# Performance work log

Hardware: AMD Instinct MI355X
Metric: run time of the kernel (lower is better)

Reference implementation:

```python
import jax, jax.numpy as jnp
import numpy as np

S = 1024        # img_size
RADIUS = 512    # number of radial bins
WEIGHT = 1.0


def _bin_idx():
    # Matches torch.meshgrid(arange(-s/2, s/2), ..., indexing='ij') with +0.5 offsets.
    xs = jnp.arange(-S / 2, S / 2, dtype=jnp.float32)
    d = jnp.sqrt((xs[:, None] + 0.5) ** 2 + (xs[None, :] + 0.5) ** 2)  # [S, S]
    # Bin edges are integers 0..RADIUS, so mask (d>=r)&(d<r+1) == (floor(d)==r).
    idx = jnp.floor(d).astype(jnp.int32)
    # Pixels with d >= RADIUS fall in no mask -> overflow bucket RADIUS (dropped later).
    return jnp.where(d < RADIUS, idx, RADIUS).reshape(-1)  # [S*S]


def _power_spec(image):
    ft = jnp.fft.fft2(image)                 # [B, C, S, S] complex
    return jnp.fft.fftshift(jnp.abs(ft) ** 2, axes=(-2, -1))


def _radial_power_spec(ps2d, idx):
    B, C = ps2d.shape[0], ps2d.shape[1]
    flat = ps2d.reshape(B * C, S * S)
    # Histogram reduction: O(S*S) instead of the original O(RADIUS*S*S) dense mask multiply.
    seg = jax.vmap(lambda v: jax.ops.segment_sum(v, idx, num_segments=RADIUS + 1))(flat)
    rad = seg[:, :RADIUS] / (S * S)          # mean over (H, W), drop overflow bucket
    return rad.reshape(B, C, RADIUS).sum(axis=1)  # sum over channel dim


def setup_inputs() -> dict:
    key = jax.random.key(0)
    k1, k2 = jax.random.split(key)
    output = jax.random.normal(k1, (16, 1, S, S), dtype=jnp.float32)
    target = jax.random.normal(k2, (16, 1, S, S), dtype=jnp.float32)
    return {"output": output, "target": target}


def reference(output, target):
    idx = _bin_idx()
    ps_out = _radial_power_spec(_power_spec(output), idx)   # [B, RADIUS]
    ps_tgt = _radial_power_spec(_power_spec(target), idx)   # [B, RADIUS]
    return jnp.mean(jnp.abs(ps_out - ps_tgt)) * WEIGHT
```

## Files before the change

### kernel.cpp

```cpp
#include <hip/hip_runtime.h>
#include <math.h>

#define S 1024
#define RADIUS 512
#define NIMG 32
#define PBX 129

__device__ __forceinline__ float2 cmul(float2 a, float2 b) {
    return make_float2(a.x * b.x - a.y * b.y, a.x * b.y + a.y * b.x);
}
__device__ __forceinline__ float2 cadd(float2 a, float2 b) { return make_float2(a.x + b.x, a.y + b.y); }
__device__ __forceinline__ float2 csub(float2 a, float2 b) { return make_float2(a.x - b.x, a.y - b.y); }

__device__ const float2 C16[8] = {
    {1.0f, 0.0f},
    {0.92387953251128674f, -0.38268343236508978f},
    {0.70710678118654757f, -0.70710678118654746f},
    {0.38268343236508984f, -0.92387953251128674f},
    {0.0f, -1.0f},
    {-0.38268343236508973f, -0.92387953251128674f},
    {-0.70710678118654746f, -0.70710678118654757f},
    {-0.92387953251128663f, -0.38268343236508989f},
};
__device__ const float2 C8T[4] = {
    {1.0f, 0.0f},
    {0.70710678118654757f, -0.70710678118654746f},
    {0.0f, -1.0f},
    {-0.70710678118654746f, -0.70710678118654757f},
};
__device__ const float2 W512T[8] = {
    {1.0f, 0.0f},
    {0.99992470183914454f, -0.012271538285719925f},
    {0.99969881869620425f, -0.024541228522912288f},
    {0.99932238458834954f, -0.036807222941358832f},
    {0.99879545620517241f, -0.049067674327418015f},
    {0.99811811290014918f, -0.061320736302208578f},
    {0.99729045667869021f, -0.073564563599667426f},
    {0.99631261218277800f, -0.085797312344439894f},
};
__device__ const float2 W64T[8] = {
    {1.0f, 0.0f},
    {0.99518472667219693f, -0.098017140329560604f},
    {0.98078528040323044f, -0.19509032201612825f},
    {0.95694033573220886f, -0.29028467725446233f},
    {0.92387953251128674f, -0.38268343236508978f},
    {0.88192126434835505f, -0.47139673682599764f},
    {0.83146961230254524f, -0.55557023301960218f},
    {0.77301045336273699f, -0.63439328416364549f},
};
__device__ const float2 W128P[8] = {
    {1.0f, 0.0f},
    {0.99879545620517241f, -0.049067674327418015f},
    {0.99518472667219693f, -0.098017140329560604f},
    {0.98917650996478101f, -0.14673047445536175f},
    {0.98078528040323044f, -0.19509032201612825f},
    {0.97003125319454397f, -0.24298017990326390f},
    {0.95694033573220886f, -0.29028467725446233f},
    {0.94154406518302081f, -0.33688985339222005f},
};
__device__ const float2 W1024P[8] = {
    {1.0f, 0.0f},
    {0.99998117528260111f, -0.0061358846491544753f},
    {0.99992470183914454f, -0.012271538285719925f},
    {0.99983058179582340f, -0.018406729905804820f},
    {0.99969881869620425f, -0.024541228522912288f},
    {0.99952941750109314f, -0.030674803176636626f},
    {0.99932238458834954f, -0.036807222941358832f},
    {0.99907772775264536f, -0.042938256934940820f},
};

__device__ __forceinline__ void fft16(float2 r[16], float2 T) {
    float2 tc[8];
    #pragma unroll
    for (int u = 0; u < 8; ++u) tc[u] = cmul(T, C16[u]);
    #pragma unroll
    for (int u = 0; u < 8; ++u) {
        float2 a = r[u], b = r[u + 8];
        r[u] = cadd(a, b);
        r[u + 8] = cmul(csub(a, b), tc[u]);
    }
    T = cmul(T, T);
    #pragma unroll
    for (int u = 0; u < 4; ++u) tc[u] = cmul(T, C16[2 * u]);
    #pragma unroll
    for (int g = 0; g < 2; ++g)
        #pragma unroll
        for (int u = 0; u < 4; ++u) {
            int lo = g * 8 + u;
            float2 a = r[lo], b = r[lo + 4];
            r[lo] = cadd(a, b);
            r[lo + 4] = cmul(csub(a, b), tc[u]);
        }
    T = cmul(T, T);
    #pragma unroll
    for (int u = 0; u < 2; ++u) tc[u] = cmul(T, C16[4 * u]);
    #pragma unroll
    for (int g = 0; g < 4; ++g)
        #pragma unroll
        for (int u = 0; u < 2; ++u) {
            int lo = g * 4 + u;
            float2 a = r[lo], b = r[lo + 2];
            r[lo] = cadd(a, b);
            r[lo + 2] = cmul(csub(a, b), tc[u]);
        }
    T = cmul(T, T);
    #pragma unroll
    for (int g = 0; g < 8; ++g) {
        int lo = g * 2;
        float2 a = r[lo], b = r[lo + 1];
        r[lo] = cadd(a, b);
        r[lo + 1] = cmul(csub(a, b), T);
    }
}

__device__ __forceinline__ void fft8(float2 r[8], float2 T) {
    float2 tc[4];
    #pragma unroll
    for (int u = 0; u < 4; ++u) tc[u] = cmul(T, C8T[u]);
    #pragma unroll
    for (int u = 0; u < 4; ++u) {
        float2 a = r[u], b = r[u + 4];
        r[u] = cadd(a, b);
        r[u + 4] = cmul(csub(a, b), tc[u]);
    }
    T = cmul(T, T);
    #pragma unroll
    for (int u = 0; u < 2; ++u) tc[u] = cmul(T, C8T[2 * u]);
    #pragma unroll
    for (int g = 0; g < 2; ++g)
        #pragma unroll
        for (int u = 0; u < 2; ++u) {
            int lo = g * 4 + u;
            float2 a = r[lo], b = r[lo + 2];
            r[lo] = cadd(a, b);
            r[lo + 2] = cmul(csub(a, b), tc[u]);
        }
    T = cmul(T, T);
    #pragma unroll
    for (int g = 0; g < 4; ++g) {
        int lo = g * 2;
        float2 a = r[lo], b = r[lo + 1];
        r[lo] = cadd(a, b);
        r[lo + 1] = cmul(csub(a, b), T);
    }
}

__device__ __forceinline__ void fft_last2(float2 r[16], int c) {
    #pragma unroll
    for (int m = 0; m < 16; ++m) {
        float vx = __shfl_xor(r[m].x, 2, 64);
        float vy = __shfl_xor(r[m].y, 2, 64);
        if (c & 2) {
            float dx = vx - r[m].x, dy = vy - r[m].y;
            if (c & 1) { r[m].x = dy; r[m].y = -dx; }
            else       { r[m].x = dx; r[m].y = dy; }
        } else {
            r[m].x += vx; r[m].y += vy;
        }
    }
    #pragma unroll
    for (int m = 0; m < 16; ++m) {
        float vx = __shfl_xor(r[m].x, 1, 64);
        float vy = __shfl_xor(r[m].y, 1, 64);
        if (c & 1) { r[m].x = vx - r[m].x; r[m].y = vy - r[m].y; }
        else       { r[m].x += vx; r[m].y += vy; }
    }
}

__device__ __forceinline__ int A1x(int n) {
    int j = n >> 6;
    return (n & ~63) | ((n & 63) ^ (j << 2));
}

__device__ __forceinline__ int bitrev3(int x) {
    return ((x & 1) << 2) | (x & 2) | ((x >> 2) & 1);
}

__global__ __launch_bounds__(512)
void fft_rows(const float* __restrict__ outp, const float* __restrict__ tgtp,
              float2* __restrict__ WpT, int imgBase) {
    __shared__ float2 buf[8 * 1024];
    const int t = threadIdx.x;
    const int w = t >> 6, tau = t & 63;
    const int yy = blockIdx.x * 8 + w;
    const int i = blockIdx.y, g = imgBase + i;
    const float* img = (g < 16 ? outp : tgtp) + (size_t)(g & 15) * S * S;
    const float* r0 = img + (size_t)(2 * yy) * S;
    const float* r1 = r0 + S;

    float2 r[16];
    #pragma unroll
    for (int j = 0; j < 16; ++j) r[j] = make_float2(r0[64 * j + tau], r1[64 * j + tau]);

    float2 T = cmul(W128P[tau >> 3], W1024P[tau & 7]);
    fft16(r, T);

    float2* mybuf = buf + (w << 10);
    #pragma unroll
    for (int j = 0; j < 16; ++j) mybuf[A1x(64 * j + tau)] = r[j];
    const int b = tau >> 2, c = tau & 3;
    #pragma unroll
    for (int m = 0; m < 16; ++m) r[m] = mybuf[(b << 6) + 4 * (m ^ b) + c];

    fft16(r, W64T[c]);
    fft_last2(r, c);

    #pragma unroll
    for (int m = 0; m < 16; ++m) {
        int n = (b << 6) + 4 * m + c;
        int k = (int)(__brev((unsigned)n) >> 22);
        mybuf[k ^ (w << 1)] = r[m];
    }
    __syncthreads();

    const int yy0 = blockIdx.x * 8;
    float2* dst = WpT + (size_t)i * 512 * 1024;
    #pragma unroll
    for (int q = 0; q < 16; ++q) {
        int idx = q * 512 + t;
        int uu = idx >> 3, wv = idx & 7;
        float2 val = buf[(wv << 10) | (uu ^ (wv << 1))];
        dst[(size_t)uu * 512 + yy0 + wv] = val;
    }
}

__global__ __launch_bounds__(512, 4)
void fft_cols_bin2(const float2* __restrict__ WpT, float* __restrict__ partial, int imgBase) {
    __shared__ float2 tbuf[8 * 512];
    __shared__ float pref[512];
    __shared__ float cws[8];
    __shared__ float cwx[8];
    const int t = threadIdx.x;
    const int w = t >> 6, tau = t & 63;
    const int i = blockIdx.y, g = imgBase + i;
    const int l = w >> 1;
    const int u = blockIdx.x * 4 + l;
    const int setb = w & 1;
    const bool active = (u <= 512);

    const int b3 = tau >> 3, lam = tau & 7;
    float2 X[8];
    float2* mb = tbuf + (w << 9);

    if (active) {
        const float2* Wimg = WpT + (size_t)i * 512 * 1024;
        const int mu = (1024 - u) & 1023;
        const float2* rowA = Wimg + (size_t)u * 512;
        const float2* rowM = Wimg + (size_t)mu * 512;

        #pragma unroll
        for (int j = 0; j < 8; ++j) {
            float2 A = rowA[64 * j + tau];
            float2 M = rowM[64 * j + tau];
            X[j] = (setb == 0)
                 ? make_float2(0.5f * (A.x + M.x), 0.5f * (A.y - M.y))
                 : make_float2(0.5f * (A.y + M.y), 0.5f * (M.x - A.x));
        }

        fft8(X, cmul(W64T[b3], W512T[lam]));

        #pragma unroll
        for (int j = 0; j < 8; ++j) mb[(j << 6) | (tau ^ (j << 3) ^ j)] = X[j];
        #pragma unroll
        for (int c = 0; c < 8; ++c) X[c] = mb[(b3 << 6) | (((c ^ b3) << 3) | (lam ^ b3))];

        fft8(X, W64T[lam]);

        #pragma unroll
        for (int c = 0; c < 8; ++c) mb[(b3 << 6) | (((c ^ b3) << 3) | (lam ^ b3))] = X[c];
        #pragma unroll
        for (int d = 0; d < 8; ++d) X[d] = mb[(b3 << 6) | (((lam ^ b3) << 3) | (d ^ b3))];

        fft8(X, make_float2(1.0f, 0.0f));

        const int base9 = 8 * bitrev3(lam) + bitrev3(b3);
        #pragma unroll
        for (int d = 0; d < 8; ++d) {
            mb[(bitrev3(d) << 6) + base9] = X[d];
        }
    }
    __syncthreads();

    float p[8];
    if (active) {
        const float2* b0 = tbuf + ((w & ~1) << 9);
        const float2* b1 = tbuf + ((w | 1) << 9);
        const float2 Wtau = cmul(W128P[tau >> 3], W1024P[tau & 7]);
        #pragma unroll
        for (int m = 0; m < 8; ++m) {
            const int f = tau + 64 * m;
            float2 x0 = b0[f];
            float2 x1 = b1[f];
            float2 Wf = cmul(Wtau, C16[m]);
            float2 wx = cmul(Wf, x1);
            float2 G = (setb == 0) ? cadd(x0, wx)
                                   : csub(x0, wx);
            p[m] = G.x * G.x + G.y * G.y;
        }
    }
    __syncthreads();

    float* Prow = (float*)tbuf;
    if (active) {
        #pragma unroll
        for (int m = 0; m < 8; ++m) {
            const int v = tau + 64 * m + (setb << 9);
            Prow[(l << 10) + v] = p[m];
        }
    }
    __syncthreads();

    const int r = t;
    const float r2  = (float)(r * r);
    const float r12 = (float)((r + 1) * (r + 1));
    float acc = 0.0f;

    for (int rowi = 0; rowi < 8; ++rowi) {
        const int ll = rowi >> 1;
        const int mir = rowi & 1;
        const int uu = blockIdx.x * 4 + ll;
        const bool valid = (uu <= 512) && (!mir || (uu >= 1 && uu <= 511));
        float F = 0.0f;
        if (valid) {
            const float* PR = Prow + (ll << 10);
            F = mir ? (PR[t + 1] + PR[(1024 - t) & 1023])
                    : (PR[t] + PR[1023 - t]);
        }
        float s = F;
        #pragma unroll
        for (int off = 1; off < 64; off <<= 1) {
            float n = __shfl_up(s, off, 64);
            if (tau >= off) s += n;
        }
        pref[t] = s;
        if (tau == 63) cws[w] = s;
        __syncthreads();
        if (t < 8) {
            float x = 0.0f;
            #pragma unroll
            for (int j = 0; j < 8; ++j) {
                if (j < t) x += cws[j];
            }
            cwx[t] = x;
        }
        __syncthreads();
        if (valid) {
            const float cuv = mir ? ((float)uu - 0.5f)
                                  : ((uu < 512) ? ((float)uu + 0.5f) : 511.5f);
            const float cu2 = cuv * cuv;
            const float Bv = r12 - cu2;
            if (Bv > 0.0f) {
                const float Av = r2 - cu2;
                float cvlo = (Av > 0.0f) ? sqrtf(Av) : 0.0f;
                float cvhi = sqrtf(Bv);
                int vlo = (int)ceilf(cvlo - 0.5f);
                int vhi = (int)ceilf(cvhi - 0.5f);
                if (vhi > 512) vhi = 512;
                if (vlo < 0) vlo = 0;
                if (vhi > vlo) {
                    float hi = pref[vhi - 1] + cwx[(vhi - 1) >> 6];
                    float lo = (vlo > 0) ? (pref[vlo - 1] + cwx[(vlo - 1) >> 6]) : 0.0f;
                    acc += hi - lo;
                }
            }
        }
        __syncthreads();
    }
    partial[(((size_t)g * PBX) + blockIdx.x) * 512 + t] = acc;
}

__global__ __launch_bounds__(512)
void reduce_partials(const float* __restrict__ partial, float* __restrict__ rad) {
    const int g = blockIdx.x;
    const int t = threadIdx.x;
    const float* p = partial + (size_t)g * PBX * 512;
    float s = 0.0f;
    for (int b = 0; b < PBX; ++b) s += p[(size_t)b * 512 + t];
    rad[(size_t)g * 512 + t] = s;
}

__global__ __launch_bounds__(256)
void final_loss(const float* __restrict__ rad, float* __restrict__ out) {
    __shared__ float red[256];
    const int t = threadIdx.x;
    float acc = 0.0f;
    for (int i = t; i < 16 * RADIUS; i += 256) {
        int bb = i >> 9;
        int rr = i & (RADIUS - 1);
        float o = rad[(size_t)bb * RADIUS + rr];
        float gg = rad[(size_t)(bb + 16) * RADIUS + rr];
        acc += fabsf(o - gg);
    }
    red[t] = acc;
    __syncthreads();
    for (int off = 128; off > 0; off >>= 1) {
        if (t < off) red[t] += red[t + off];
        __syncthreads();
    }
    if (t == 0) {
        out[0] = red[0] / ((float)S * (float)S) / (16.0f * (float)RADIUS);
    }
}

extern "C" void kernel_launch(void* const* d_in, const int* in_sizes, int n_in,
                              void* d_out, int out_size, void* d_ws, size_t ws_size,
                              hipStream_t stream) {
    const float* outp = (const float*)d_in[0];
    const float* tgtp = (const float*)d_in[1];
    float* dout = (float*)d_out;

    char* ws = (char*)d_ws;
    float* rad = (float*)ws;
    const size_t partBytes = (size_t)NIMG * PBX * 512 * sizeof(float);
    float* partial = (float*)(ws + 65536);
    float2* WpT = (float2*)(ws + 65536 + partBytes);
    const size_t perImg = (size_t)512 * 1024 * sizeof(float2);
    size_t used = 65536 + partBytes;
    size_t avail = (ws_size > used) ? (ws_size - used) : 0;
    int chunk = (int)(avail / perImg);
    if (chunk > NIMG) chunk = NIMG;
    if (chunk < 1) chunk = 1;

    for (int base = 0; base < NIMG; base += chunk) {
        int c = (NIMG - base < chunk) ? (NIMG - base) : chunk;
        fft_rows<<<dim3(64, c), 512, 0, stream>>>(outp, tgtp, WpT, base);
        fft_cols_bin2<<<dim3(PBX, c), 512, 0, stream>>>(WpT, partial, base);
    }

    reduce_partials<<<NIMG, 512, 0, stream>>>(partial, rad);
    final_loss<<<1, 256, 0, stream>>>(rad, dout);
}
```

Measured before the change: 171.5 us.

## Halve fft_rows shared memory via two-phase transposes to raise occupancy

Shrinks the row-FFT kernel's shared buffer from 8K to 4K float2 by performing both in-kernel transposes in two halves, and declares four blocks per CU in launch bounds. The intent is to lift occupancy limited by shared-memory size and improve latency hiding. It adds extra barriers and an extra 8-element register array, which may increase register pressure or cause spills under the tighter launch bound.

```diff
diff --git a/kernel.cpp b/kernel.cpp
--- a/kernel.cpp
+++ b/kernel.cpp
@@ -167,19 +167,14 @@
     }
 }
 
-__device__ __forceinline__ int A1x(int n) {
-    int j = n >> 6;
-    return (n & ~63) | ((n & 63) ^ (j << 2));
-}
-
 __device__ __forceinline__ int bitrev3(int x) {
     return ((x & 1) << 2) | (x & 2) | ((x >> 2) & 1);
 }
 
-__global__ __launch_bounds__(512)
+__global__ __launch_bounds__(512, 4)
 void fft_rows(const float* __restrict__ outp, const float* __restrict__ tgtp,
               float2* __restrict__ WpT, int imgBase) {
-    __shared__ float2 buf[8 * 1024];
+    __shared__ float2 buf[4096];
     const int t = threadIdx.x;
     const int w = t >> 6, tau = t & 63;
     const int yy = blockIdx.x * 8 + w;
@@ -192,35 +187,54 @@
     #pragma unroll
     for (int j = 0; j < 16; ++j) r[j] = make_float2(r0[64 * j + tau], r1[64 * j + tau]);
 
-    float2 T = cmul(W128P[tau >> 3], W1024P[tau & 7]);
-    fft16(r, T);
-
-    float2* mybuf = buf + (w << 10);
-    #pragma unroll
-    for (int j = 0; j < 16; ++j) mybuf[A1x(64 * j + tau)] = r[j];
+    fft16(r, cmul(W128P[tau >> 3], W1024P[tau & 7]));
+
+    float2* wb = buf + (w << 9);
     const int b = tau >> 2, c = tau & 3;
-    #pragma unroll
-    for (int m = 0; m < 16; ++m) r[m] = mybuf[(b << 6) + 4 * (m ^ b) + c];
+    float2 ex[8];
+    #pragma unroll
+    for (int j = 0; j < 8; ++j) wb[(j << 6) | (tau ^ (j << 2))] = r[j];
+    if (b < 8) {
+        #pragma unroll
+        for (int m = 0; m < 8; ++m)  r[m]      = wb[((b & 7) << 6) + 4 * ((m ^ b) & 15) + c];
+        #pragma unroll
+        for (int m = 8; m < 16; ++m) ex[m - 8] = wb[((b & 7) << 6) + 4 * ((m ^ b) & 15) + c];
+    }
+    #pragma unroll
+    for (int j = 8; j < 16; ++j) wb[((j & 7) << 6) | (tau ^ (j << 2))] = r[j];
+    if (b >= 8) {
+        #pragma unroll
+        for (int m = 0; m < 8; ++m)  r[m]      = wb[((b & 7) << 6) + 4 * ((m ^ b) & 15) + c];
+        #pragma unroll
+        for (int m = 8; m < 16; ++m) ex[m - 8] = wb[((b & 7) << 6) + 4 * ((m ^ b) & 15) + c];
+    }
+    #pragma unroll
+    for (int m = 8; m < 16; ++m) r[m] = ex[m - 8];
 
     fft16(r, W64T[c]);
     fft_last2(r, c);
 
-    #pragma unroll
-    for (int m = 0; m < 16; ++m) {
-        int n = (b << 6) + 4 * m + c;
-        int k = (int)(__brev((unsigned)n) >> 22);
-        mybuf[k ^ (w << 1)] = r[m];
-    }
-    __syncthreads();
-
     const int yy0 = blockIdx.x * 8;
     float2* dst = WpT + (size_t)i * 512 * 1024;
     #pragma unroll
-    for (int q = 0; q < 16; ++q) {
-        int idx = q * 512 + t;
-        int uu = idx >> 3, wv = idx & 7;
-        float2 val = buf[(wv << 10) | (uu ^ (wv << 1))];
-        dst[(size_t)uu * 512 + yy0 + wv] = val;
+    for (int h = 0; h < 2; ++h) {
+        if ((c & 1) == h) {
+            #pragma unroll
+            for (int m = 0; m < 16; ++m) {
+                int n = (b << 6) + 4 * m + c;
+                int kh = (int)(__brev((unsigned)n) >> 22) & 511;
+                buf[(w << 9) | (kh ^ (w << 1))] = r[m];
+            }
+        }
+        __syncthreads();
+        #pragma unroll
+        for (int q = 0; q < 8; ++q) {
+            int idx = q * 512 + t;
+            int uu = idx >> 3, wv = idx & 7;
+            float2 val = buf[(wv << 9) | (uu ^ (wv << 1))];
+            dst[(size_t)(uu + (h << 9)) * 512 + yy0 + wv] = val;
+        }
+        __syncthreads();
     }
 }
 
```

Result: no change. 174.9 us (+2.0%).
